# Kernel tuning notes

Hardware: AMD Instinct MI355X
Metric: run time of the kernel (lower is better)

The kernel has to match this reference:

```python
import jax, jax.numpy as jnp
import numpy as np

N_PATCHES = 16
PATCH = 128
RECEPTIVE_FIELD = 0


def setup_inputs() -> dict:
    key = jax.random.key(0)
    k1, k2, k3, k4 = jax.random.split(key, 4)
    B, C = 8, 3
    Hl = Wl = 256
    Hh = Wh = 2048
    x_low = jax.random.normal(k1, (B, C, Hl, Wl), jnp.float32)
    x_high = jax.random.normal(k2, (B, C, Hh, Wh), jnp.float32)
    # attention must be strictly positive (log is taken)
    attention = jax.random.uniform(k3, (B, Hl, Wl), jnp.float32, minval=1e-3, maxval=1.0)
    # uniform noise for the Gumbel-max trick (torch.rand_like equivalent)
    noise_u = jax.random.uniform(k4, (B, Hl * Wl), jnp.float32, minval=1e-6, maxval=1.0 - 1e-6)
    return {"x_low": x_low, "x_high": x_high, "attention": attention, "noise_u": noise_u}


def reference(x_low, x_high, attention, noise_u):
    B, Ha, Wa = attention.shape
    # --- Gumbel-max top-k sampling without replacement ---
    logits = jnp.log(attention).reshape(B, -1)          # [B, Ha*Wa]
    z = -jnp.log(-jnp.log(noise_u))                     # Gumbel noise
    _, idx = jax.lax.top_k(logits + z, N_PATCHES)       # [B, N] flat indices
    sampled_attention = jnp.take_along_axis(attention.reshape(B, -1), idx, axis=1)  # [B, N]
    # unravel flat indices -> (row, col) in sample space
    samples = jnp.stack([idx // Wa, idx % Wa], axis=-1).astype(jnp.float32)  # [B, N, 2]

    # --- offset computation (FromTensors.patches) ---
    Hl, Wl = x_low.shape[2], x_low.shape[3]
    Hh, Wh = x_high.shape[2], x_high.shape[3]
    scale_offsets = jnp.array([Hh / Hl, Wh / Wl], jnp.float32)
    prev_patch = jnp.array([Hl - RECEPTIVE_FIELD, Wl - RECEPTIVE_FIELD], jnp.float32)
    steps = prev_patch * scale_offsets / jnp.array([Ha, Wa], jnp.float32)
    patch_f = jnp.array([PATCH, PATCH], jnp.float32)
    base_off = 0.0 if RECEPTIVE_FIELD <= 0 else RECEPTIVE_FIELD / 2.0
    offsets = jnp.round(base_off * scale_offsets + samples * steps + steps / 2.0 - patch_f / 2.0).astype(jnp.int32)  # [B, N, 2]

    # --- patch extraction with zero padding of patch_size//2 ---
    pad_const = PATCH // 2
    img = jnp.pad(x_high, ((0, 0), (0, 0), (pad_const, pad_const), (pad_const, pad_const)))  # [B,C,Hh+P,Wh+P]
    offsets = offsets + pad_const
    C = img.shape[1]

    def crop(img_b, off):  # img_b: [C,H,W], off: [2]
        return jax.lax.dynamic_slice(img_b, (0, off[0], off[1]), (C, PATCH, PATCH))

    patches = jax.vmap(lambda im, offs: jax.vmap(lambda o: crop(im, o))(offs))(img, offsets)  # [B,N,C,P,P]
    return patches, sampled_attention
```

## Files before the change

### kernel.cpp

```cpp
#include <hip/hip_runtime.h>

typedef unsigned long long u64;
typedef unsigned int u32;

#define HW 65536
#define NB 8
#define NSEL 16
#define NC 3
#define HH 2048

__device__ __forceinline__ u32 wkey(float a, float u) {
  float v = __builtin_amdgcn_logf(u);
  float w = a * __builtin_amdgcn_rcpf(-v);
  return __float_as_uint(w);
}

__device__ __forceinline__ u64 wave_max64(u64 k) {
#pragma unroll
  for (int off = 1; off < 64; off <<= 1) {
    u32 lo = __shfl_xor((u32)k, off, 64);
    u32 hi = __shfl_xor((u32)(k >> 32), off, 64);
    u64 o = ((u64)hi << 32) | lo;
    if (o > k) k = o;
  }
  return k;
}

#define CMPSWAP(a, b) { if ((b) > (a)) { u64 t_ = (a); (a) = (b); (b) = t_; } }

__global__ __launch_bounds__(256) void scan_topk(
    const float* __restrict__ att, const float* __restrict__ noise,
    u64* __restrict__ cand) {
  const int tid = threadIdx.x;
  const int lane = tid & 63;
  const int wave = tid >> 6;
  const int b = blockIdx.x >> 6;
  const int blk = blockIdx.x & 63;

  __shared__ u64 s_wtop[64];

  const int ebase = blk * 1024 + wave * 256;
  u64 k4[4];
#pragma unroll
  for (int j = 0; j < 4; j++) {
    const int e = ebase + (j << 6) + lane;
    const int gi = b * HW + e;
    k4[j] = ((u64)wkey(att[gi], noise[gi]) << 32) | (0xFFFFFFFFu - (u32)e);
  }
  CMPSWAP(k4[0], k4[1]); CMPSWAP(k4[2], k4[3]);
  CMPSWAP(k4[0], k4[2]); CMPSWAP(k4[1], k4[3]);
  CMPSWAP(k4[1], k4[2]);

#pragma unroll
  for (int r = 0; r < NSEL; r++) {
    u64 g = wave_max64(k4[0]);
    if (k4[0] == g) {
      s_wtop[wave * 16 + r] = g;
      k4[0] = k4[1]; k4[1] = k4[2]; k4[2] = k4[3]; k4[3] = 0ULL;
    }
  }
  __syncthreads();

  if (wave == 0) {
    u64 kk = s_wtop[lane];
#pragma unroll
    for (int r = 0; r < NSEL; r++) {
      u64 g = wave_max64(kk);
      if (kk == g) {
        cand[(size_t)blockIdx.x * NSEL + r] = g;
        kk = 0ULL;
      }
    }
  }
}

__global__ __launch_bounds__(256) void merge_patch(
    const float* __restrict__ xh, const float* __restrict__ att,
    const u64* __restrict__ cand, float* __restrict__ out,
    float* __restrict__ att_out) {
  const int blk = blockIdx.x;
  const int h = blk & 1;
  const int pairc = blk >> 1;
  const int c = pairc % 3;
  const int bn = pairc / 3;
  const int b = bn >> 4;
  const int n = bn & 15;
  const int tid = threadIdx.x;
  const int lane = tid & 63;
  const int wave = tid >> 6;

  __shared__ int s_idx[NSEL];

  if (wave == 0) {
    const u64* cb = cand + (size_t)(b * 64 + lane) * NSEL;
    u64 lst[NSEL];
#pragma unroll
    for (int j = 0; j < NSEL; j++) lst[j] = cb[j];
    u64 won = 0ULL;
#pragma unroll
    for (int r = 0; r < NSEL; r++) {
      u64 g = wave_max64(lst[0]);
      if (lane == r) won = g;
      if (lst[0] == g) {
#pragma unroll
        for (int i = 0; i < NSEL - 1; i++) lst[i] = lst[i + 1];
        lst[NSEL - 1] = 0ULL;
      }
    }
    if (lane < NSEL) {
      u32 e = 0xFFFFFFFFu - (u32)(won & 0xFFFFFFFFu);
      s_idx[lane] = (int)e;
      if (pairc == b * 48 && h == 0)
        att_out[b * NSEL + lane] = att[b * HW + (int)e];
    }
  }
  __syncthreads();

  const int e = s_idx[n];
  const int sr = e >> 8;
  const int sc = e & 255;
  const int r0 = sr * 8 - 60 + h * 64;
  const int c0 = sc * 8 - 60;
  const float* src = xh + ((size_t)(b * NC + c) << 22);
  float* dst = out + (size_t)pairc * (128 * 128) + (size_t)h * (64 * 128);

#pragma unroll
  for (int i = tid; i < 64 * 32; i += 256) {
    const int pr = i >> 5;
    const int q = i & 31;
    const int r = r0 + pr;
    const int cc = c0 + (q << 2);
    float4 v = make_float4(0.f, 0.f, 0.f, 0.f);
    if ((u32)r < (u32)HH && (u32)cc < (u32)HH) {
      v = *reinterpret_cast<const float4*>(src + ((size_t)r << 11) + cc);
    }
    *reinterpret_cast<float4*>(dst + ((size_t)i << 2)) = v;
  }
}

extern "C" void kernel_launch(void* const* d_in, const int* in_sizes, int n_in,
                              void* d_out, int out_size, void* d_ws, size_t ws_size,
                              hipStream_t stream) {
  (void)in_sizes; (void)n_in; (void)out_size; (void)ws_size;
  const float* x_high = (const float*)d_in[1];
  const float* att    = (const float*)d_in[2];
  const float* noise  = (const float*)d_in[3];
  float* out = (float*)d_out;
  float* att_out = out + (size_t)NB * NSEL * NC * 128 * 128;

  u64* cand = (u64*)d_ws;

  scan_topk<<<dim3(NB * 64), dim3(256), 0, stream>>>(att, noise, cand);
  merge_patch<<<dim3(NB * NSEL * NC * 2), dim3(256), 0, stream>>>(
      x_high, att, cand, out, att_out);
}
```

Measured before the change: 32.17 us.

## Split final top-k merge into its own kernel and vectorize scan loads

Each patch-copy block used to redo the full 64x16 candidate merge. That merge now runs once per batch in a small separate kernel, which writes the selected indices to workspace. The copy kernel reads those indices and is split into quarter-patch blocks, giving twice as many blocks. The scan kernel now loads attention and noise as float4, so each lane's four elements are contiguous. This removes redundant merge work but adds a third kernel launch and a serial dependency step.

Result: no change. 32.77 us (+1.9%).

```diff
diff --git a/kernel.cpp b/kernel.cpp
--- a/kernel.cpp
+++ b/kernel.cpp
@@ -40,12 +40,16 @@
   __shared__ u64 s_wtop[64];
 
   const int ebase = blk * 1024 + wave * 256;
+  const float4 av = *reinterpret_cast<const float4*>(att + b * HW + ebase + (lane << 2));
+  const float4 uv = *reinterpret_cast<const float4*>(noise + b * HW + ebase + (lane << 2));
+
   u64 k4[4];
-#pragma unroll
-  for (int j = 0; j < 4; j++) {
-    const int e = ebase + (j << 6) + lane;
-    const int gi = b * HW + e;
-    k4[j] = ((u64)wkey(att[gi], noise[gi]) << 32) | (0xFFFFFFFFu - (u32)e);
+  {
+    const u32 e0 = (u32)(ebase + (lane << 2));
+    k4[0] = ((u64)wkey(av.x, uv.x) << 32) | (0xFFFFFFFFu - e0);
+    k4[1] = ((u64)wkey(av.y, uv.y) << 32) | (0xFFFFFFFFu - (e0 + 1));
+    k4[2] = ((u64)wkey(av.z, uv.z) << 32) | (0xFFFFFFFFu - (e0 + 2));
+    k4[3] = ((u64)wkey(av.w, uv.w) << 32) | (0xFFFFFFFFu - (e0 + 3));
   }
   CMPSWAP(k4[0], k4[1]); CMPSWAP(k4[2], k4[3]);
   CMPSWAP(k4[0], k4[2]); CMPSWAP(k4[1], k4[3]);
@@ -74,58 +78,53 @@
   }
 }
 
-__global__ __launch_bounds__(256) void merge_patch(
-    const float* __restrict__ xh, const float* __restrict__ att,
-    const u64* __restrict__ cand, float* __restrict__ out,
-    float* __restrict__ att_out) {
-  const int blk = blockIdx.x;
-  const int h = blk & 1;
-  const int pairc = blk >> 1;
+__global__ __launch_bounds__(64) void final_merge(
+    const u64* __restrict__ cand, const float* __restrict__ att,
+    int* __restrict__ idx_sel, float* __restrict__ att_out) {
+  const int b = blockIdx.x;
+  const int lane = threadIdx.x;
+
+  const u64* cb = cand + (size_t)(b * 64 + lane) * NSEL;
+  u64 lst[NSEL];
+#pragma unroll
+  for (int j = 0; j < NSEL; j++) lst[j] = cb[j];
+  u64 won = 0ULL;
+#pragma unroll
+  for (int r = 0; r < NSEL; r++) {
+    u64 g = wave_max64(lst[0]);
+    if (lane == r) won = g;
+    if (lst[0] == g) {
+#pragma unroll
+      for (int i = 0; i < NSEL - 1; i++) lst[i] = lst[i + 1];
+      lst[NSEL - 1] = 0ULL;
+    }
+  }
+  if (lane < NSEL) {
+    u32 e = 0xFFFFFFFFu - (u32)(won & 0xFFFFFFFFu);
+    idx_sel[b * NSEL + lane] = (int)e;
+    att_out[b * NSEL + lane] = att[b * HW + (int)e];
+  }
+}
+
+__global__ __launch_bounds__(256) void patch_extract(
+    const float* __restrict__ xh, const int* __restrict__ idx_sel,
+    float* __restrict__ out) {
+  const int q4 = blockIdx.x & 3;
+  const int pairc = blockIdx.x >> 2;
   const int c = pairc % 3;
   const int bn = pairc / 3;
   const int b = bn >> 4;
-  const int n = bn & 15;
   const int tid = threadIdx.x;
-  const int lane = tid & 63;
-  const int wave = tid >> 6;
 
-  __shared__ int s_idx[NSEL];
-
-  if (wave == 0) {
-    const u64* cb = cand + (size_t)(b * 64 + lane) * NSEL;
-    u64 lst[NSEL];
-#pragma unroll
-    for (int j = 0; j < NSEL; j++) lst[j] = cb[j];
-    u64 won = 0ULL;
-#pragma unroll
-    for (int r = 0; r < NSEL; r++) {
-      u64 g = wave_max64(lst[0]);
-      if (lane == r) won = g;
-      if (lst[0] == g) {
-#pragma unroll
-        for (int i = 0; i < NSEL - 1; i++) lst[i] = lst[i + 1];
-        lst[NSEL - 1] = 0ULL;
-      }
-    }
-    if (lane < NSEL) {
-      u32 e = 0xFFFFFFFFu - (u32)(won & 0xFFFFFFFFu);
-      s_idx[lane] = (int)e;
-      if (pairc == b * 48 && h == 0)
-        att_out[b * NSEL + lane] = att[b * HW + (int)e];
-    }
-  }
-  __syncthreads();
-
-  const int e = s_idx[n];
-  const int sr = e >> 8;
-  const int sc = e & 255;
-  const int r0 = sr * 8 - 60 + h * 64;
-  const int c0 = sc * 8 - 60;
+  const int e = idx_sel[bn];
+  const int r0 = (e >> 8) * 8 - 60 + q4 * 32;
+  const int c0 = (e & 255) * 8 - 60;
   const float* src = xh + ((size_t)(b * NC + c) << 22);
-  float* dst = out + (size_t)pairc * (128 * 128) + (size_t)h * (64 * 128);
+  float4* dst = (float4*)out + (size_t)pairc * 4096 + (size_t)q4 * 1024;
 
 #pragma unroll
-  for (int i = tid; i < 64 * 32; i += 256) {
+  for (int it = 0; it < 4; it++) {
+    const int i = it * 256 + tid;
     const int pr = i >> 5;
     const int q = i & 31;
     const int r = r0 + pr;
@@ -134,7 +133,7 @@
     if ((u32)r < (u32)HH && (u32)cc < (u32)HH) {
       v = *reinterpret_cast<const float4*>(src + ((size_t)r << 11) + cc);
     }
-    *reinterpret_cast<float4*>(dst + ((size_t)i << 2)) = v;
+    dst[i] = v;
   }
 }
 
@@ -148,9 +147,12 @@
   float* out = (float*)d_out;
   float* att_out = out + (size_t)NB * NSEL * NC * 128 * 128;
 
-  u64* cand = (u64*)d_ws;
+  char* ws = (char*)d_ws;
+  u64* cand    = (u64*)ws;
+  int* idx_sel = (int*)(ws + 512 * NSEL * 8);
 
   scan_topk<<<dim3(NB * 64), dim3(256), 0, stream>>>(att, noise, cand);
-  merge_patch<<<dim3(NB * NSEL * NC * 2), dim3(256), 0, stream>>>(
-      x_high, att, cand, out, att_out);
+  final_merge<<<dim3(NB), dim3(64), 0, stream>>>(cand, att, idx_sel, att_out);
+  patch_extract<<<dim3(NB * NSEL * NC * 4), dim3(256), 0, stream>>>(
+      x_high, idx_sel, out);
 }
```
